# Optimization experiments

Measured on AMD Instinct MI355X. Metric: run time of the kernel, lower is better.

## Reference

```python
import jax, jax.numpy as jnp
import numpy as np

N_EMBD = 1024
N_HEAD = 16
B, T = 2, 2048


def setup_inputs() -> dict:
    key = jax.random.key(0)
    k1, k2, k3 = jax.random.split(key, 3)
    scale = 1.0 / np.sqrt(N_EMBD)
    x = jax.random.normal(k1, (B, T, N_EMBD), dtype=jnp.float32)
    W_qkv = jax.random.normal(k2, (N_EMBD, 3 * N_EMBD), dtype=jnp.float32) * scale
    b_qkv = jnp.zeros((3 * N_EMBD,), dtype=jnp.float32)
    W_proj = jax.random.normal(k3, (N_EMBD, N_EMBD), dtype=jnp.float32) * scale
    b_proj = jnp.zeros((N_EMBD,), dtype=jnp.float32)
    return {"x": x, "W_qkv": W_qkv, "b_qkv": b_qkv, "W_proj": W_proj, "b_proj": b_proj}


def reference(x, W_qkv, b_qkv, W_proj, b_proj):
    Bx, Tx, C = x.shape
    H = N_HEAD
    D = C // H  # head_size
    qkv = x @ W_qkv + b_qkv  # [B,T,3C]
    Q, K, V = jnp.split(qkv, 3, axis=2)
    # [B,T,C] -> [B,H,T,D]
    Q = Q.reshape(Bx, Tx, H, D).transpose(0, 2, 1, 3)
    K = K.reshape(Bx, Tx, H, D).transpose(0, 2, 1, 3)
    V = V.reshape(Bx, Tx, H, D).transpose(0, 2, 1, 3)
    scores = jnp.einsum("bhqd,bhkd->bhqk", Q, K) / jnp.sqrt(jnp.float32(D))
    causal = jnp.tril(jnp.ones((Tx, Tx), dtype=bool))
    scores = jnp.where(causal, scores, jnp.float32(-jnp.inf))
    weights = jax.nn.softmax(scores, axis=-1)
    out = jnp.einsum("bhqk,bhkd->bhqd", weights, V)  # [B,H,T,D]
    out = out.transpose(0, 2, 1, 3).reshape(Bx, Tx, C)
    return out @ W_proj + b_proj
```

## Files before the change

### kernel.cpp

```cpp
#include <hip/hip_runtime.h>
#include <hip/hip_bf16.h>
#include <math.h>

#define BB 2
#define TT 2048
#define CC 1024
#define HH 16
#define DD 64
#define C3 3072
#define BT 4096

typedef __attribute__((ext_vector_type(8))) short short8;
typedef __attribute__((ext_vector_type(8))) unsigned short ushort8;
typedef __attribute__((ext_vector_type(4))) unsigned short ushort4v;
typedef __attribute__((ext_vector_type(4))) float floatx4;

__device__ __forceinline__ unsigned short f2b(float f) {
    union { float f; unsigned int u; } v; v.f = f;
    unsigned int u = v.u;
    unsigned int r = (u + 0x7fffu + ((u >> 16) & 1u)) >> 16;
    return (unsigned short)r;
}
__device__ __forceinline__ unsigned short f2b_fast(float f) {
    unsigned int u = __builtin_bit_cast(unsigned int, f);
    return (unsigned short)((u + 0x8000u) >> 16);
}

__device__ __forceinline__ void store_out(unsigned short* p, float v) { *p = f2b(v); }
__device__ __forceinline__ void store_out(float* p, float v) { *p = v; }

__device__ __forceinline__ void async16(const unsigned short* g, unsigned short* lds) {
    __builtin_amdgcn_global_load_lds(
        (const __attribute__((address_space(1))) unsigned int*)g,
        (__attribute__((address_space(3))) unsigned int*)lds, 16, 0, 0);
}

__global__ __launch_bounds__(256) void prep_kernel(
    const float* __restrict__ x, unsigned short* __restrict__ xb,
    const float* __restrict__ Wqkv, const float* __restrict__ Wproj,
    unsigned short* __restrict__ Wqkv_t, unsigned short* __restrict__ Wproj_t)
{
    __shared__ float tile[64 * 65];
    const int tid = threadIdx.x;
    const int bid = blockIdx.x;

    if (bid < 2048) {
        int i = bid * 256 + tid;
        const float4 v0 = *(const float4*)&x[(size_t)i * 8];
        const float4 v1 = *(const float4*)&x[(size_t)i * 8 + 4];
        ushort8 pk;
        pk[0] = f2b(v0.x); pk[1] = f2b(v0.y); pk[2] = f2b(v0.z); pk[3] = f2b(v0.w);
        pk[4] = f2b(v1.x); pk[5] = f2b(v1.y); pk[6] = f2b(v1.z); pk[7] = f2b(v1.w);
        *(ushort8*)&xb[(size_t)i * 8] = pk;
        return;
    }

    const int xt = bid - 2048;
    const int cxt = xt & 63;
    const int r0  = (xt >> 6) * 64;
    const float* src; unsigned short* dst; int Ccols, c0;
    if (cxt < 48) { src = Wqkv;  dst = Wqkv_t;  Ccols = C3; c0 = cxt * 64; }
    else          { src = Wproj; dst = Wproj_t; Ccols = CC; c0 = (cxt - 48) * 64; }
#pragma unroll
    for (int it = 0; it < 4; it++) {
        int idx = it * 256 + tid;
        int row = idx >> 4;
        int c4  = idx & 15;
        float4 v = *(const float4*)&src[(size_t)(r0 + row) * Ccols + c0 + c4 * 4];
        tile[row * 65 + c4 * 4 + 0] = v.x;
        tile[row * 65 + c4 * 4 + 1] = v.y;
        tile[row * 65 + c4 * 4 + 2] = v.z;
        tile[row * 65 + c4 * 4 + 3] = v.w;
    }
    __syncthreads();
#pragma unroll
    for (int it = 0; it < 2; it++) {
        int idx = it * 256 + tid;
        int orow = idx >> 3;
        int o8   = idx & 7;
        ushort8 pk;
#pragma unroll
        for (int j = 0; j < 8; j++) pk[j] = f2b(tile[(o8 * 8 + j) * 65 + orow]);
        *(ushort8*)&dst[(size_t)(c0 + orow) * CC + r0 + o8 * 8] = pk;
    }
}

template <typename OUT_T, bool FRAG>
__global__ __launch_bounds__(256) void gemm_bt_kernel(
    const unsigned short* __restrict__ A, const unsigned short* __restrict__ Bm,
    const float* __restrict__ bias, OUT_T* __restrict__ Cmat,
    unsigned short* __restrict__ Qf, unsigned short* __restrict__ Kf,
    unsigned short* __restrict__ Vf,
    int M, int N, int K, float qscale)
{
    __shared__ __align__(16) unsigned short sA[128 * 64];
    __shared__ __align__(16) unsigned short sB[128 * 64];

    const int tid = threadIdx.x;
    const int lane16 = tid & 15, quad = (tid & 63) >> 4;
    const int w = tid >> 6;
    const int wm = w >> 1, wn = w & 1;
    const int m0 = blockIdx.y * 128, n0 = blockIdx.x * 128;
    const int lx = lane16 & 7;

    floatx4 acc[4][4] = {};

    for (int kt = 0; kt < K; kt += 64) {
#pragma unroll
        for (int it = 0; it < 4; it++) {
            int idx = it * 256 + tid;
            int row = idx >> 3;
            int c8m = (idx & 7) ^ (row & 7);
            int wslot = it * 256 + (tid & 192);
            async16(&A[(size_t)(m0 + row) * K + kt + c8m * 8], &sA[wslot * 8]);
            async16(&Bm[(size_t)(n0 + row) * K + kt + c8m * 8], &sB[wslot * 8]);
        }
        __syncthreads();
#pragma unroll
        for (int ks = 0; ks < 64; ks += 32) {
            const int slot = ((ks >> 3) + quad) ^ lx;
            short8 af[4], bf[4];
#pragma unroll
            for (int t = 0; t < 4; t++) {
                af[t] = *(const short8*)&sA[(wm * 64 + t * 16 + lane16) * 64 + slot * 8];
                bf[t] = *(const short8*)&sB[(wn * 64 + t * 16 + lane16) * 64 + slot * 8];
            }
#pragma unroll
            for (int mt = 0; mt < 4; mt++)
#pragma unroll
                for (int nt = 0; nt < 4; nt++)
                    acc[mt][nt] = __builtin_amdgcn_mfma_f32_16x16x32_bf16(
                        af[mt], bf[nt], acc[mt][nt], 0, 0, 0);
        }
        __syncthreads();
    }

#pragma unroll
    for (int mt = 0; mt < 4; mt++) {
#pragma unroll
        for (int nt = 0; nt < 4; nt++) {
            int col = n0 + wn * 64 + nt * 16 + lane16;
            float bv = bias[col];
            int row0 = m0 + wm * 64 + mt * 16 + quad * 4;
            if (!FRAG) {
#pragma unroll
                for (int r = 0; r < 4; r++)
                    store_out(&Cmat[(size_t)(row0 + r) * N + col], acc[mt][nt][r] + bv);
            } else {
                const int breg = row0 >> 11;
                const int tok0 = row0 & (TT - 1);
                if (col < CC) {
                    int h = col >> 6, d = col & 63;
                    int bh = breg * HH + h;
                    size_t base = ((size_t)(bh * 128 + (tok0 >> 4)) * 2 + (d >> 5)) * 512
                                + ((d >> 3) & 3) * 128 + (tok0 & 15) * 8 + (d & 7);
#pragma unroll
                    for (int r = 0; r < 4; r++)
                        Qf[base + r * 8] = f2b((acc[mt][nt][r] + bv) * qscale);
                } else if (col < 2 * CC) {
                    int c = col - CC;
                    int h = c >> 6, d = c & 63;
                    int bh = breg * HH + h;
                    size_t base = ((size_t)(bh * 128 + (tok0 >> 4)) * 2 + (d >> 5)) * 512
                                + ((d >> 3) & 3) * 128 + (tok0 & 15) * 8 + (d & 7);
#pragma unroll
                    for (int r = 0; r < 4; r++)
                        Kf[base + r * 8] = f2b(acc[mt][nt][r] + bv);
                } else {
                    int c = col - 2 * CC;
                    int h = c >> 6, d = c & 63;
                    int bh = breg * HH + h;
                    size_t base = ((size_t)(bh * 64 + (tok0 >> 5)) * 4 + (d >> 4)) * 512
                                + (((tok0 >> 2) & 3) * 16 + (d & 15)) * 8
                                + ((tok0 >> 4) & 1) * 4;
                    ushort4v pk;
#pragma unroll
                    for (int r = 0; r < 4; r++) pk[r] = f2b(acc[mt][nt][r] + bv);
                    *(ushort4v*)&Vf[base] = pk;
                }
            }
        }
    }
}

__global__ __launch_bounds__(64) void attn_mfma_kernel(
    const unsigned short* __restrict__ Qf, const unsigned short* __restrict__ Kf,
    const unsigned short* __restrict__ Vf, unsigned short* __restrict__ att)
{
    const int l = threadIdx.x;
    const int lane16 = l & 15, quad = l >> 4;
    const int bh = blockIdx.x;
    const int b = bh >> 4, h = bh & 15;

    const int y = blockIdx.y;
    const int gcu = y & 7, s = y >> 3;
    const int p = 8 * s + ((s & 1) ? (7 - gcu) : gcu);
    const int q0 = p * 64;

    const unsigned short* Qb = Qf + (size_t)bh * 131072 + l * 8;
    const unsigned short* Kb = Kf + (size_t)bh * 131072 + l * 8;
    const unsigned short* Vb = Vf + (size_t)bh * 131072 + l * 8;

    short8 qf[4][2];
#pragma unroll
    for (int qg = 0; qg < 4; qg++)
#pragma unroll
        for (int dc = 0; dc < 2; dc++)
            qf[qg][dc] = *(const short8*)&Qb[(size_t)((p * 4 + qg) * 2 + dc) * 512];

    floatx4 O[4][4] = {};
    float ps[4] = {0.f, 0.f, 0.f, 0.f};
    short8 kfa[8], kfb[8];

    const int ntiles = p + 1;
#pragma unroll
    for (int i = 0; i < 8; i++)
        kfa[i] = *(const short8*)&Kb[(size_t)i * 512];

    auto body = [&](int t, short8 (&KC)[8], short8 (&KN)[8]) {
        const bool last = (t == ntiles - 1);

        short8 vf[8];
#pragma unroll
        for (int i = 0; i < 8; i++)
            vf[i] = *(const short8*)&Vb[(size_t)(t * 8 + i) * 512];

        if (t + 1 < ntiles) {
#pragma unroll
            for (int i = 0; i < 8; i++)
                KN[i] = *(const short8*)&Kb[(size_t)((t + 1) * 8 + i) * 512];
        }

        short8 pa[4][2];
#pragma unroll
        for (int nt = 0; nt < 4; nt++) {
#pragma unroll
            for (int qg = 0; qg < 4; qg++) {
                floatx4 s4 = {};
                s4 = __builtin_amdgcn_mfma_f32_16x16x32_bf16(KC[nt * 2 + 0], qf[qg][0], s4, 0, 0, 0);
                s4 = __builtin_amdgcn_mfma_f32_16x16x32_bf16(KC[nt * 2 + 1], qf[qg][1], s4, 0, 0, 0);
#pragma unroll
                for (int r = 0; r < 4; r++) {
                    float v = s4[r];
                    if (last) {
                        if (nt * 16 + quad * 4 + r > qg * 16 + lane16) v = -1e30f;
                    }
                    float pe = __builtin_amdgcn_exp2f(v);
                    ps[qg] += pe;
                    pa[qg][nt >> 1][(nt & 1) * 4 + r] = (short)f2b_fast(pe);
                }
            }
        }

#pragma unroll
        for (int kc = 0; kc < 2; kc++)
#pragma unroll
            for (int dt = 0; dt < 4; dt++)
#pragma unroll
                for (int qg = 0; qg < 4; qg++)
                    O[qg][dt] = __builtin_amdgcn_mfma_f32_16x16x32_bf16(
                        pa[qg][kc], vf[kc * 4 + dt], O[qg][dt], 0, 0, 0);
    };

    int t = 0;
    while (true) {
        body(t, kfa, kfb); if (++t == ntiles) break;
        body(t, kfb, kfa); if (++t == ntiles) break;
    }

#pragma unroll
    for (int qg = 0; qg < 4; qg++) {
        ps[qg] += __shfl_xor(ps[qg], 16, 64);
        ps[qg] += __shfl_xor(ps[qg], 32, 64);
    }

    unsigned short* ob = att + ((size_t)(b * TT) + q0) * CC + h * DD;
#pragma unroll
    for (int qg = 0; qg < 4; qg++)
#pragma unroll
        for (int r = 0; r < 4; r++) {
            float rl = 1.0f / __shfl(ps[qg], quad * 4 + r, 16);
            int q = qg * 16 + quad * 4 + r;
#pragma unroll
            for (int dt = 0; dt < 4; dt++)
                ob[(size_t)q * CC + dt * 16 + lane16] = f2b(O[qg][dt][r] * rl);
        }
}

extern "C" void kernel_launch(void* const* d_in, const int* in_sizes, int n_in,
                              void* d_out, int out_size, void* d_ws, size_t ws_size,
                              hipStream_t stream) {
    const float* x     = (const float*)d_in[0];
    const float* Wqkv  = (const float*)d_in[1];
    const float* bqkv  = (const float*)d_in[2];
    const float* Wproj = (const float*)d_in[3];
    const float* bproj = (const float*)d_in[4];
    float* out = (float*)d_out;

    const size_t FRAG_ELEMS = (size_t)128 * 2 * 512;
    unsigned short* xb      = (unsigned short*)d_ws;
    unsigned short* Qf      = xb + (size_t)BT * CC;
    unsigned short* Kf      = Qf + (size_t)BB * HH * FRAG_ELEMS;
    unsigned short* Vf      = Kf + (size_t)BB * HH * FRAG_ELEMS;
    unsigned short* Wqkv_t  = Vf + (size_t)BB * HH * FRAG_ELEMS;
    unsigned short* Wproj_t = Wqkv_t + (size_t)C3 * CC;
    unsigned short* att_b   = Wproj_t + (size_t)CC * CC;

    prep_kernel<<<3072, 256, 0, stream>>>(x, xb, Wqkv, Wproj, Wqkv_t, Wproj_t);

    {
        dim3 grid(C3 / 128, BT / 128);
        gemm_bt_kernel<unsigned short, true><<<grid, 256, 0, stream>>>(
            xb, Wqkv_t, bqkv, (unsigned short*)nullptr, Qf, Kf, Vf,
            BT, C3, CC, 0.125f * 1.44269504f);
    }
    {
        dim3 grid(BB * HH, 32);
        attn_mfma_kernel<<<grid, 64, 0, stream>>>(Qf, Kf, Vf, att_b);
    }
    {
        dim3 grid(CC / 128, BT / 128);
        gemm_bt_kernel<float, false><<<grid, 256, 0, stream>>>(
            att_b, Wproj_t, bproj, out, nullptr, nullptr, nullptr,
            BT, CC, CC, 1.0f);
    }
}
```

Baseline: 194.8 us.

## Split attention KV tiles across two waves and combine partials via LDS

The attention kernel now runs two wavefronts per block, each handling alternating key/value tiles (stride 2) for the same 64-query block. Each wave accumulates partial O and row sums, exchanges half of them through shared memory, and writes out two of the four query groups. This doubles the parallelism per query block to hide memory latency and raise occupancy, at the cost of an LDS reduction, a barrier and extra shared memory. Softmax without a running max stays valid because partial sums combine additively.

```diff
diff --git a/kernel.cpp b/kernel.cpp
--- a/kernel.cpp
+++ b/kernel.cpp
@@ -183,11 +183,15 @@
     }
 }
 
-__global__ __launch_bounds__(64) void attn_mfma_kernel(
+__global__ __launch_bounds__(128) void attn_mfma_kernel(
     const unsigned short* __restrict__ Qf, const unsigned short* __restrict__ Kf,
     const unsigned short* __restrict__ Vf, unsigned short* __restrict__ att)
 {
-    const int l = threadIdx.x;
+    __shared__ __align__(16) float comb[2 * 9 * 256];
+
+    const int tid = threadIdx.x;
+    const int l = tid & 63;
+    const int w = tid >> 6;
     const int lane16 = l & 15, quad = l >> 4;
     const int bh = blockIdx.x;
     const int b = bh >> 4, h = bh & 15;
@@ -213,9 +217,6 @@
     short8 kfa[8], kfb[8];
 
     const int ntiles = p + 1;
-#pragma unroll
-    for (int i = 0; i < 8; i++)
-        kfa[i] = *(const short8*)&Kb[(size_t)i * 512];
 
     auto body = [&](int t, short8 (&KC)[8], short8 (&KN)[8]) {
         const bool last = (t == ntiles - 1);
@@ -225,10 +226,10 @@
         for (int i = 0; i < 8; i++)
             vf[i] = *(const short8*)&Vb[(size_t)(t * 8 + i) * 512];
 
-        if (t + 1 < ntiles) {
+        if (t + 2 < ntiles) {
 #pragma unroll
             for (int i = 0; i < 8; i++)
-                KN[i] = *(const short8*)&Kb[(size_t)((t + 1) * 8 + i) * 512];
+                KN[i] = *(const short8*)&Kb[(size_t)((t + 2) * 8 + i) * 512];
         }
 
         short8 pa[4][2];
@@ -262,10 +263,15 @@
                         pa[qg][kc], vf[kc * 4 + dt], O[qg][dt], 0, 0, 0);
     };
 
-    int t = 0;
-    while (true) {
-        body(t, kfa, kfb); if (++t == ntiles) break;
-        body(t, kfb, kfa); if (++t == ntiles) break;
+    int t = w;
+    if (t < ntiles) {
+#pragma unroll
+        for (int i = 0; i < 8; i++)
+            kfa[i] = *(const short8*)&Kb[(size_t)(t * 8 + i) * 512];
+        while (true) {
+            body(t, kfa, kfb); t += 2; if (t >= ntiles) break;
+            body(t, kfb, kfa); t += 2; if (t >= ntiles) break;
+        }
     }
 
 #pragma unroll
@@ -274,9 +280,35 @@
         ps[qg] += __shfl_xor(ps[qg], 32, 64);
     }
 
+    {
+        float* mine = comb + w * (9 * 256);
+        const int wbase = w ? 0 : 2;
+#pragma unroll
+        for (int qg = 0; qg < 2; qg++)
+#pragma unroll
+            for (int dt = 0; dt < 4; dt++)
+                *(floatx4*)&mine[(qg * 4 + dt) * 256 + l * 4] = O[wbase + qg][dt];
+        floatx4 ps4;
+        ps4[0] = ps[0]; ps4[1] = ps[1]; ps4[2] = ps[2]; ps4[3] = ps[3];
+        *(floatx4*)&mine[8 * 256 + l * 4] = ps4;
+    }
+    __syncthreads();
+    const int outbase = w * 2;
+    {
+        const float* other = comb + (1 - w) * (9 * 256);
+#pragma unroll
+        for (int qg = 0; qg < 2; qg++)
+#pragma unroll
+            for (int dt = 0; dt < 4; dt++)
+                O[outbase + qg][dt] += *(const floatx4*)&other[(qg * 4 + dt) * 256 + l * 4];
+        floatx4 op = *(const floatx4*)&other[8 * 256 + l * 4];
+#pragma unroll
+        for (int j = 0; j < 4; j++) ps[j] += op[j];
+    }
+
     unsigned short* ob = att + ((size_t)(b * TT) + q0) * CC + h * DD;
 #pragma unroll
-    for (int qg = 0; qg < 4; qg++)
+    for (int qg = outbase; qg < outbase + 2; qg++)
 #pragma unroll
         for (int r = 0; r < 4; r++) {
             float rl = 1.0f / __shfl(ps[qg], quad * 4 + r, 16);
@@ -316,7 +348,7 @@
     }
     {
         dim3 grid(BB * HH, 32);
-        attn_mfma_kernel<<<grid, 64, 0, stream>>>(Qf, Kf, Vf, att_b);
+        attn_mfma_kernel<<<grid, 128, 0, stream>>>(Qf, Kf, Vf, att_b);
     }
     {
         dim3 grid(CC / 128, BT / 128);
```

New measurement: 194.5 us. About the same (-0.1%).

## Split attention work into 16-query-row wavefronts for more parallelism

Applied to the files above, without the earlier changes.

Each attention block now handles 16 query rows instead of 64, which quadruples the grid to 128 blocks per head. The interleaved tile-order remapping across CUs is dropped and launch bounds gain an occupancy hint. The smaller per-wave register footprint is meant to raise occupancy and help load balance under the causal mask. In exchange, every K/V tile is reloaded four times as often, so global and L2 traffic per useful MFMA goes up.

```diff
diff --git a/kernel.cpp b/kernel.cpp
--- a/kernel.cpp
+++ b/kernel.cpp
@@ -183,7 +183,7 @@
     }
 }
 
-__global__ __launch_bounds__(64) void attn_mfma_kernel(
+__global__ __launch_bounds__(64, 4) void attn_mfma_kernel(
     const unsigned short* __restrict__ Qf, const unsigned short* __restrict__ Kf,
     const unsigned short* __restrict__ Vf, unsigned short* __restrict__ att)
 {
@@ -191,28 +191,22 @@
     const int lane16 = l & 15, quad = l >> 4;
     const int bh = blockIdx.x;
     const int b = bh >> 4, h = bh & 15;
-
-    const int y = blockIdx.y;
-    const int gcu = y & 7, s = y >> 3;
-    const int p = 8 * s + ((s & 1) ? (7 - gcu) : gcu);
-    const int q0 = p * 64;
+    const int j = blockIdx.y;
 
     const unsigned short* Qb = Qf + (size_t)bh * 131072 + l * 8;
     const unsigned short* Kb = Kf + (size_t)bh * 131072 + l * 8;
     const unsigned short* Vb = Vf + (size_t)bh * 131072 + l * 8;
 
-    short8 qf[4][2];
-#pragma unroll
-    for (int qg = 0; qg < 4; qg++)
-#pragma unroll
-        for (int dc = 0; dc < 2; dc++)
-            qf[qg][dc] = *(const short8*)&Qb[(size_t)((p * 4 + qg) * 2 + dc) * 512];
-
-    floatx4 O[4][4] = {};
-    float ps[4] = {0.f, 0.f, 0.f, 0.f};
+    short8 qf0 = *(const short8*)&Qb[(size_t)(j * 2 + 0) * 512];
+    short8 qf1 = *(const short8*)&Qb[(size_t)(j * 2 + 1) * 512];
+
+    floatx4 O[4] = {};
+    float ps = 0.f;
     short8 kfa[8], kfb[8];
 
-    const int ntiles = p + 1;
+    const int ntiles = (j >> 2) + 1;
+    const int qrow = j * 16 + lane16;
+
 #pragma unroll
     for (int i = 0; i < 8; i++)
         kfa[i] = *(const short8*)&Kb[(size_t)i * 512];
@@ -231,24 +225,22 @@
                 KN[i] = *(const short8*)&Kb[(size_t)((t + 1) * 8 + i) * 512];
         }
 
-        short8 pa[4][2];
+        short8 pa[2];
 #pragma unroll
         for (int nt = 0; nt < 4; nt++) {
-#pragma unroll
-            for (int qg = 0; qg < 4; qg++) {
-                floatx4 s4 = {};
-                s4 = __builtin_amdgcn_mfma_f32_16x16x32_bf16(KC[nt * 2 + 0], qf[qg][0], s4, 0, 0, 0);
-                s4 = __builtin_amdgcn_mfma_f32_16x16x32_bf16(KC[nt * 2 + 1], qf[qg][1], s4, 0, 0, 0);
-#pragma unroll
-                for (int r = 0; r < 4; r++) {
-                    float v = s4[r];
-                    if (last) {
-                        if (nt * 16 + quad * 4 + r > qg * 16 + lane16) v = -1e30f;
-                    }
-                    float pe = __builtin_amdgcn_exp2f(v);
-                    ps[qg] += pe;
-                    pa[qg][nt >> 1][(nt & 1) * 4 + r] = (short)f2b_fast(pe);
+            floatx4 s4 = {};
+            s4 = __builtin_amdgcn_mfma_f32_16x16x32_bf16(KC[nt * 2 + 0], qf0, s4, 0, 0, 0);
+            s4 = __builtin_amdgcn_mfma_f32_16x16x32_bf16(KC[nt * 2 + 1], qf1, s4, 0, 0, 0);
+#pragma unroll
+            for (int r = 0; r < 4; r++) {
+                float v = s4[r];
+                if (last) {
+                    int key = t * 64 + nt * 16 + quad * 4 + r;
+                    if (key > qrow) v = -1e30f;
                 }
+                float pe = __builtin_amdgcn_exp2f(v);
+                ps += pe;
+                pa[nt >> 1][(nt & 1) * 4 + r] = (short)f2b_fast(pe);
             }
         }
 
@@ -256,10 +248,8 @@
         for (int kc = 0; kc < 2; kc++)
 #pragma unroll
             for (int dt = 0; dt < 4; dt++)
-#pragma unroll
-                for (int qg = 0; qg < 4; qg++)
-                    O[qg][dt] = __builtin_amdgcn_mfma_f32_16x16x32_bf16(
-                        pa[qg][kc], vf[kc * 4 + dt], O[qg][dt], 0, 0, 0);
+                O[dt] = __builtin_amdgcn_mfma_f32_16x16x32_bf16(
+                    pa[kc], vf[kc * 4 + dt], O[dt], 0, 0, 0);
     };
 
     int t = 0;
@@ -268,23 +258,18 @@
         body(t, kfb, kfa); if (++t == ntiles) break;
     }
 
-#pragma unroll
-    for (int qg = 0; qg < 4; qg++) {
-        ps[qg] += __shfl_xor(ps[qg], 16, 64);
-        ps[qg] += __shfl_xor(ps[qg], 32, 64);
-    }
-
-    unsigned short* ob = att + ((size_t)(b * TT) + q0) * CC + h * DD;
-#pragma unroll
-    for (int qg = 0; qg < 4; qg++)
-#pragma unroll
-        for (int r = 0; r < 4; r++) {
-            float rl = 1.0f / __shfl(ps[qg], quad * 4 + r, 16);
-            int q = qg * 16 + quad * 4 + r;
-#pragma unroll
-            for (int dt = 0; dt < 4; dt++)
-                ob[(size_t)q * CC + dt * 16 + lane16] = f2b(O[qg][dt][r] * rl);
-        }
+    ps += __shfl_xor(ps, 16, 64);
+    ps += __shfl_xor(ps, 32, 64);
+
+    unsigned short* ob = att + ((size_t)(b * TT) + j * 16) * CC + h * DD;
+#pragma unroll
+    for (int r = 0; r < 4; r++) {
+        float rl = 1.0f / __shfl(ps, quad * 4 + r, 16);
+        int q = quad * 4 + r;
+#pragma unroll
+        for (int dt = 0; dt < 4; dt++)
+            ob[(size_t)q * CC + dt * 16 + lane16] = f2b(O[dt][r] * rl);
+    }
 }
 
 extern "C" void kernel_launch(void* const* d_in, const int* in_sizes, int n_in,
@@ -315,7 +300,7 @@
             BT, C3, CC, 0.125f * 1.44269504f);
     }
     {
-        dim3 grid(BB * HH, 32);
+        dim3 grid(BB * HH, 128);
         attn_mfma_kernel<<<grid, 64, 0, stream>>>(Qf, Kf, Vf, att_b);
     }
     {
```

Result: slower. 234.3 us (+20.3%).
